# Kernel tuning notes

Hardware: AMD Instinct MI355X
Metric: run time of the kernel (lower is better)

## Reference

```python
import jax, jax.numpy as jnp
import numpy as np

B, H, W = 4, 128, 128
THRESHOLD = 0.1      # hard-coded in chamfer_distance_batch
CHUNK = 2048         # row-chunk size for the online-min over the distance matrix
BIG = 1e9            # masks out inactive columns in the min-reduction
EMPTY_CHD = 1e6      # sentinel when either point set is empty (matches torch code)
EPS = 1e-12          # sqrt clamp for numerical safety


def setup_inputs() -> dict:
    key = jax.random.key(0)
    k1, k2 = jax.random.split(key)
    batch1 = jax.random.normal(k1, (B, H, W), dtype=jnp.float32)
    batch2 = jax.random.normal(k2, (B, H, W), dtype=jnp.float32)
    return {"batch1": batch1, "batch2": batch2}


def _chamfer(batch1, batch2):
    Bn, Hn, Wn = batch1.shape
    HW = Hn * Wn
    w1 = jax.nn.relu(batch1 - THRESHOLD).reshape(Bn, HW)   # [B, HW]
    w2 = jax.nn.relu(batch2 - THRESHOLD).reshape(Bn, HW)
    gy, gx = jnp.meshgrid(jnp.arange(Hn), jnp.arange(Wn), indexing='ij')
    coords = jnp.stack([gy, gx], axis=-1).reshape(HW, 2).astype(jnp.float32)  # [HW, 2]
    # torch code multiplies coords by the relu'd weights BEFORE cdist (quirk kept)
    c1 = coords[None, :, :] * w1[:, :, None]               # [B, HW, 2]
    c2 = coords[None, :, :] * w2[:, :, None]
    m1 = w1 > 0                                            # active-point masks
    m2 = w2 > 0

    def directed(cf, mf, ct, mt):
        # mean over active rows of min distance to active columns, chunked
        ct_sq = jnp.sum(ct * ct, axis=-1)                  # [HW]

        def chunk_min(cc):                                 # cc: [CHUNK, 2]
            # |a-b|^2 = |a|^2 + |b|^2 - 2 a.b  (GEMM form)
            d2 = (jnp.sum(cc * cc, axis=-1)[:, None]
                  + ct_sq[None, :]
                  - 2.0 * cc @ ct.T)                       # [CHUNK, HW]
            d = jnp.sqrt(jnp.maximum(d2, EPS))
            return jnp.min(jnp.where(mt[None, :], d, BIG), axis=1)  # [CHUNK]

        mins = jax.lax.map(chunk_min, cf.reshape(-1, CHUNK, 2)).reshape(-1)  # [HW]
        n = jnp.sum(mf)
        return jnp.sum(mins * mf) / jnp.maximum(n, 1)

    def per_image(c1b, m1b, c2b, m2b):
        chd = directed(c1b, m1b, c2b, m2b) + directed(c2b, m2b, c1b, m1b)
        nonempty = (jnp.sum(m1b) > 0) & (jnp.sum(m2b) > 0)
        return jnp.where(nonempty, chd, jnp.asarray(EMPTY_CHD, chd.dtype))

    return jax.vmap(per_image)(c1, m1, c2, m2)   # [B]


def reference(batch1, batch2):
    return _chamfer(batch1, batch2)
```

## Files before the change

### kernel.cpp

```cpp
#include <hip/hip_runtime.h>
#include <math.h>


#define B_ 4
#define HW_ 16384
#define THRESH 0.1f
#define BIGF 1e30f
#define EPS_ 1e-12f

#define SEGCAP 4096
#define NSEG 4
#define NBIN 1024
#define BINSCALE 1.0f
#define BINW 1.0f
#define RG 128
#define NW 8
#define AWIN 768
#define PD_NGRP 128

__global__ __launch_bounds__(1024)
void compact_kernel(const float* __restrict__ in1, const float* __restrict__ in2,
                    int* __restrict__ segcounts, float4* __restrict__ pts,
                    uint4* __restrict__ minarr4, int* __restrict__ histG) {
    int seg = blockIdx.x, combo = blockIdx.y;
    int b = combo >> 1, s = combo & 1;
    int tid = threadIdx.x, lane = tid & 63, wid = tid >> 6;
    const float* in = s ? in2 : in1;
    int ibase = seg * SEGCAP + tid * 4;
    float4 v = ((const float4*)(in + b * HW_))[(unsigned)ibase >> 2];
    float w0 = v.x - THRESH, w1 = v.y - THRESH, w2 = v.z - THRESH, w3 = v.w - THRESH;
    int a0 = w0 > 0.f, a1 = w1 > 0.f, a2 = w2 > 0.f, a3 = w3 > 0.f;

    unsigned int bb = __float_as_uint(BIGF);
    minarr4[(unsigned)(combo * HW_ + ibase) >> 2] = make_uint4(bb, bb, bb, bb);

    __shared__ int hist[NBIN];
    if (tid < NBIN) hist[tid] = 0;

    int c = a0 + a1 + a2 + a3;
    int incl = c;
#pragma unroll
    for (int o = 1; o < 64; o <<= 1) {
        int x = __shfl_up(incl, o, 64);
        if (lane >= o) incl += x;
    }
    int wexcl = incl - c;
    __shared__ int wtot[16], wpre[17];
    if (lane == 63) wtot[wid] = incl;
    __syncthreads();
    if (tid == 0) {
        int run = 0;
#pragma unroll
        for (int ww = 0; ww < 16; ++ww) { wpre[ww] = run; run += wtot[ww]; }
        wpre[16] = run;
    }
    __syncthreads();
    int off = wpre[wid] + wexcl;
    float4* dst = pts + combo * HW_ + seg * SEGCAP;
    float wv[4] = {w0, w1, w2, w3};
    int   av[4] = {a0, a1, a2, a3};
#pragma unroll
    for (int u = 0; u < 4; ++u) {
        if (av[u]) {
            int i = ibase + u;
            float qx = (float)(i >> 7) * wv[u];
            float qy = (float)(i & 127) * wv[u];
            float zz = qx * qx + qy * qy;
            dst[off] = make_float4(qx, qy, zz, 0.0f);
            int bin = min(NBIN - 1, (int)(sqrtf(zz) * BINSCALE));
            atomicAdd(&hist[bin], 1);
            ++off;
        }
    }
    if (tid == 0) segcounts[combo * 4 + seg] = wpre[16];
    __syncthreads();
    if (tid < NBIN)
        histG[(combo * NSEG + seg) * NBIN + tid] = hist[tid];
}

__global__ __launch_bounds__(1024)
void scatter_kernel(const int* __restrict__ segcounts, const float4* __restrict__ pts,
                    const int* __restrict__ histG, float4* __restrict__ sorted,
                    int* __restrict__ binstartG) {
    int seg = blockIdx.x, combo = blockIdx.y;
    int tid = threadIdx.x;
    __shared__ int h[NSEG][NBIN];
    __shared__ int sc[NBIN];
    __shared__ int cur[NBIN];
    for (int i = tid; i < NSEG * NBIN; i += 1024)
        h[i >> 10][i & (NBIN - 1)] = histG[combo * NSEG * NBIN + i];
    __syncthreads();
    if (tid < NBIN) sc[tid] = h[0][tid] + h[1][tid] + h[2][tid] + h[3][tid];
    __syncthreads();
#pragma unroll
    for (int o = 1; o < NBIN; o <<= 1) {
        int v = (tid < NBIN && tid >= o) ? sc[tid - o] : 0;
        __syncthreads();
        if (tid < NBIN) sc[tid] += v;
        __syncthreads();
    }
    if (tid < NBIN) {
        int tot = h[0][tid] + h[1][tid] + h[2][tid] + h[3][tid];
        int excl = sc[tid] - tot;
        int o2 = excl;
        for (int s2 = 0; s2 < seg; ++s2) o2 += h[s2][tid];
        cur[tid] = o2;
        if (seg == 0) binstartG[combo * (NBIN + 1) + tid] = excl;
    }
    if (seg == 0 && tid == 0)
        binstartG[combo * (NBIN + 1) + NBIN] = sc[NBIN - 1];
    __syncthreads();
    int c = segcounts[combo * 4 + seg];
    const float4* src = pts + combo * HW_ + seg * SEGCAP;
    for (int i = tid; i < c; i += 1024) {
        float4 p = src[i];
        int bin = min(NBIN - 1, (int)(sqrtf(p.z) * BINSCALE));
        int idx = atomicAdd(&cur[bin], 1);
        sorted[(size_t)combo * HW_ + idx] =
            make_float4(p.x, p.y, p.z, __uint_as_float((unsigned)(seg * SEGCAP + i)));
    }
}

__global__ __launch_bounds__(512, 4)
void pdist_kernel(const float4* __restrict__ sorted, const int* __restrict__ binstart,
                  unsigned int* __restrict__ minarr) {
    int grp = blockIdx.x, combo = blockIdx.y;
    int tid = threadIdx.x, lane = tid & 63, w = tid >> 6;
    int tc = combo ^ 1;
    int n_from = binstart[combo * (NBIN + 1) + NBIN];
    int n_to   = binstart[tc * (NBIN + 1) + NBIN];
    if (n_from <= 0 || n_to <= 0) return;
    int rbase = grp * RG;
    if (rbase >= n_from) return;

    const float4* __restrict__ rows = sorted + (size_t)combo * HW_;
    const float4* __restrict__ cols = sorted + (size_t)tc * HW_;

    int r0 = rbase + lane, r1 = rbase + 64 + lane;
    bool v0 = r0 < n_from, v1 = r1 < n_from;
    float4 P0 = rows[min(r0, n_from - 1)];
    float4 P1 = rows[min(r1, n_from - 1)];
    float npx0 = -2.0f * P0.x, npy0 = -2.0f * P0.y, p20 = P0.z;
    float npx1 = -2.0f * P1.x, npy1 = -2.0f * P1.y, p21 = P1.z;
    unsigned int slot0 = __float_as_uint(P0.w);
    unsigned int slot1 = __float_as_uint(P1.w);
    float m0 = BIGF, m1 = BIGF;

    int blo_r = min(NBIN - 1, (int)(sqrtf(rows[rbase].z) * BINSCALE));
    int bhi_r = min(NBIN - 1, (int)(sqrtf(rows[min(rbase + RG - 1, n_from - 1)].z) * BINSCALE));
    float rho_lo = (float)blo_r * BINW;
    float rho_hi = (float)(bhi_r + 1) * BINW;

    int jmid = (binstart[tc * (NBIN + 1) + blo_r]
                + binstart[tc * (NBIN + 1) + min(bhi_r + 1, NBIN)]) >> 1;
    int aHi = min(n_to, jmid + AWIN / 2);
    int aLo = max(0, aHi - AWIN);
    aHi = min(n_to, aLo + AWIN);

    __shared__ __align__(16) float bx[NW][64], by[NW][64], bz[NW][64];
    __shared__ float mW[NW][RG];

    auto ld = [&](int jb) -> float4 {
        int j = jb + lane;
        return (j < n_to) ? cols[j] : make_float4(0.0f, 0.0f, BIGF, 0.0f);
    };
    auto proc = [&](float4 qc) {
        bx[w][lane] = qc.x; by[w][lane] = qc.y; bz[w][lane] = qc.z;
        const float4* X = (const float4*)bx[w];
        const float4* Y = (const float4*)by[w];
        const float4* Z = (const float4*)bz[w];
#pragma unroll
        for (int q4 = 0; q4 < 16; ++q4) {
            float4 qx = X[q4], qy = Y[q4], qz = Z[q4];
            float t0 = fmaf(qy.x, npy0, fmaf(qx.x, npx0, qz.x));
            float u1 = fmaf(qy.y, npy0, fmaf(qx.y, npx0, qz.y));
            m0 = fminf(m0, fminf(t0, u1));
            float u2 = fmaf(qy.z, npy0, fmaf(qx.z, npx0, qz.z));
            float u3 = fmaf(qy.w, npy0, fmaf(qx.w, npx0, qz.w));
            m0 = fminf(m0, fminf(u2, u3));
            float s0 = fmaf(qy.x, npy1, fmaf(qx.x, npx1, qz.x));
            float s1 = fmaf(qy.y, npy1, fmaf(qx.y, npx1, qz.y));
            m1 = fminf(m1, fminf(s0, s1));
            float s2 = fmaf(qy.z, npy1, fmaf(qx.z, npx1, qz.z));
            float s3 = fmaf(qy.w, npy1, fmaf(qx.w, npx1, qz.w));
            m1 = fminf(m1, fminf(s2, s3));
        }
    };

    int nbA = (aHi - aLo + 63) >> 6;
    float4 qn = (w < nbA) ? ld(aLo + (w << 6))
                          : make_float4(0.0f, 0.0f, BIGF, 0.0f);
    for (int bi = w; bi < nbA; bi += NW) {
        float4 qc = qn;
        if (bi + NW < nbA) qn = ld(aLo + ((bi + NW) << 6));
        proc(qc);
    }

    mW[w][lane] = m0; mW[w][64 + lane] = m1;
    __syncthreads();
    float c0 = mW[0][lane], c1 = mW[0][64 + lane];
#pragma unroll
    for (int ww = 1; ww < NW; ++ww) {
        c0 = fminf(c0, mW[ww][lane]);
        c1 = fminf(c1, mW[ww][64 + lane]);
    }
    float md0 = v0 ? fmaxf(c0 + p20, 0.0f) : -1.0f;
    float md1 = v1 ? fmaxf(c1 + p21, 0.0f) : -1.0f;
    float g = fmaxf(md0, md1);
#pragma unroll
    for (int o = 1; o < 64; o <<= 1) g = fmaxf(g, __shfl_xor(g, o));

    float S = sqrtf((g + 1.0f) * (1.0f / 0.99f)) * 1.001f;
    int b_lo = max(0, (int)((rho_lo - S) * BINSCALE) - 1);
    int b_hi = min(NBIN, (int)((rho_hi + S) * BINSCALE) + 2);
    int jlo2 = binstart[tc * (NBIN + 1) + b_lo];
    int jhi2 = binstart[tc * (NBIN + 1) + b_hi];

    m0 = c0; m1 = c1;
    int nbL = (max(0, aLo - jlo2) + 63) >> 6;
    int nbR = (max(0, jhi2 - aHi) + 63) >> 6;
    int nbB = nbL + nbR;
    auto jbB = [&](int bi) {
        return (bi < nbL) ? (jlo2 + (bi << 6)) : (aHi + ((bi - nbL) << 6));
    };
    qn = (w < nbB) ? ld(jbB(w)) : make_float4(0.0f, 0.0f, BIGF, 0.0f);
    for (int bi = w; bi < nbB; bi += NW) {
        float4 qc = qn;
        if (bi + NW < nbB) qn = ld(jbB(bi + NW));
        proc(qc);
    }
    __syncthreads();
    mW[w][lane] = m0; mW[w][64 + lane] = m1;
    __syncthreads();
    if (w == 0) {
        float f0 = mW[0][lane], f1 = mW[0][64 + lane];
#pragma unroll
        for (int ww = 1; ww < NW; ++ww) {
            f0 = fminf(f0, mW[ww][lane]);
            f1 = fminf(f1, mW[ww][64 + lane]);
        }
        if (v0) minarr[combo * HW_ + slot0] = __float_as_uint(fmaxf(f0 + p20, 0.0f));
        if (v1) minarr[combo * HW_ + slot1] = __float_as_uint(fmaxf(f1 + p21, 0.0f));
    }
}

__global__ void reduce_out_kernel(const int* __restrict__ segcounts,
                                  const unsigned int* __restrict__ minarr,
                                  float* __restrict__ out) {
    int b = blockIdx.x;
    int tid = threadIdx.x;
    int d = tid >> 9;
    int t = tid & 511;
    int combo = b * 2 + d;

    float acc = 0.0f;
    for (int s = 0; s < NSEG; ++s) {
        int c = segcounts[combo * 4 + s];
        const unsigned int* ma = minarr + combo * HW_ + s * SEGCAP;
        for (int r = t; r < c; r += 512)
            acc += sqrtf(fmaxf(__uint_as_float(ma[r]), EPS_));
    }
#pragma unroll
    for (int o = 32; o >= 1; o >>= 1) acc += __shfl_down(acc, o);

    __shared__ float wsum[16];
    if ((tid & 63) == 0) wsum[tid >> 6] = acc;
    __syncthreads();
    if (tid == 0) {
        float s0 = 0.0f, s1 = 0.0f;
#pragma unroll
        for (int w = 0; w < 8; ++w)  s0 += wsum[w];
#pragma unroll
        for (int w = 8; w < 16; ++w) s1 += wsum[w];
        int n0 = 0, n1 = 0;
#pragma unroll
        for (int s = 0; s < NSEG; ++s) {
            n0 += segcounts[(b * 2) * 4 + s];
            n1 += segcounts[(b * 2 + 1) * 4 + s];
        }
        out[b] = (n0 > 0 && n1 > 0)
                 ? s0 / (float)n0 + s1 / (float)n1
                 : 1.0e6f;
    }
}

extern "C" void kernel_launch(void* const* d_in, const int* in_sizes, int n_in,
                              void* d_out, int out_size, void* d_ws, size_t ws_size,
                              hipStream_t stream) {
    const float* in1 = (const float*)d_in[0];
    const float* in2 = (const float*)d_in[1];
    float* out = (float*)d_out;
    char* ws = (char*)d_ws;
    int* segcounts = (int*)ws;
    float4* pts = (float4*)(ws + 256);
    size_t minoff = 256 + (size_t)8 * HW_ * sizeof(float4);
    unsigned int* minarr = (unsigned int*)(ws + minoff);
    size_t sortoff = minoff + (size_t)8 * HW_ * sizeof(unsigned int);
    float4* sorted = (float4*)(ws + sortoff);
    size_t binoff = sortoff + (size_t)8 * HW_ * sizeof(float4);
    int* binstart = (int*)(ws + binoff);
    size_t histoff = binoff + (size_t)8 * (NBIN + 1) * sizeof(int);
    int* histG = (int*)(ws + histoff);

    hipLaunchKernelGGL(compact_kernel, dim3(NSEG, 8), dim3(1024), 0, stream,
                       in1, in2, segcounts, pts, (uint4*)minarr, histG);
    hipLaunchKernelGGL(scatter_kernel, dim3(NSEG, 8), dim3(1024), 0, stream,
                       segcounts, pts, histG, sorted, binstart);
    hipLaunchKernelGGL(pdist_kernel, dim3(PD_NGRP, 8), dim3(512), 0, stream,
                       sorted, binstart, minarr);
    hipLaunchKernelGGL(reduce_out_kernel, dim3(B_), dim3(1024), 0, stream,
                       segcounts, minarr, out);
}
```

Before: 79.07 us.

## Fuse final reduction into pdist via last-block counter; wave-shuffle scan in scatter

Removes the separate reduce_out kernel launch. Each pdist block bumps a per-batch atomic counter, and the last of that batch's 256 blocks performs the sqrt-sum and mean. The scatter kernel's shared-memory Hillis-Steele scan over 1024 bins is replaced with a wave-level shuffle scan plus a 16-entry cross-wave scan, cutting many __syncthreads. The cost is a threadfence and atomic in every pdist block, plus a serial tail where a single block per batch reduces 32K values.

```diff
diff --git a/kernel.cpp b/kernel.cpp
--- a/kernel.cpp
+++ b/kernel.cpp
@@ -81,34 +81,46 @@
 __global__ __launch_bounds__(1024)
 void scatter_kernel(const int* __restrict__ segcounts, const float4* __restrict__ pts,
                     const int* __restrict__ histG, float4* __restrict__ sorted,
-                    int* __restrict__ binstartG) {
+                    int* __restrict__ binstartG, int* __restrict__ donecnt) {
     int seg = blockIdx.x, combo = blockIdx.y;
-    int tid = threadIdx.x;
+    int tid = threadIdx.x, lane = tid & 63, wid = tid >> 6;
+    if (seg == 0 && (combo & 1) == 0 && tid == 0)
+        donecnt[combo >> 1] = 0;
     __shared__ int h[NSEG][NBIN];
-    __shared__ int sc[NBIN];
     __shared__ int cur[NBIN];
+    __shared__ int wtot[16];
     for (int i = tid; i < NSEG * NBIN; i += 1024)
         h[i >> 10][i & (NBIN - 1)] = histG[combo * NSEG * NBIN + i];
     __syncthreads();
-    if (tid < NBIN) sc[tid] = h[0][tid] + h[1][tid] + h[2][tid] + h[3][tid];
-    __syncthreads();
-#pragma unroll
-    for (int o = 1; o < NBIN; o <<= 1) {
-        int v = (tid < NBIN && tid >= o) ? sc[tid - o] : 0;
-        __syncthreads();
-        if (tid < NBIN) sc[tid] += v;
-        __syncthreads();
-    }
-    if (tid < NBIN) {
-        int tot = h[0][tid] + h[1][tid] + h[2][tid] + h[3][tid];
-        int excl = sc[tid] - tot;
+    int tot = h[0][tid] + h[1][tid] + h[2][tid] + h[3][tid];
+    int v = tot;
+#pragma unroll
+    for (int o = 1; o < 64; o <<= 1) {
+        int x = __shfl_up(v, o, 64);
+        if (lane >= o) v += x;
+    }
+    if (lane == 63) wtot[wid] = v;
+    __syncthreads();
+    if (wid == 0) {
+        int wv = (lane < 16) ? wtot[lane] : 0;
+#pragma unroll
+        for (int o = 1; o < 16; o <<= 1) {
+            int x = __shfl_up(wv, o, 64);
+            if (lane >= o) wv += x;
+        }
+        if (lane < 16) wtot[lane] = wv;
+    }
+    __syncthreads();
+    int incl = v + (wid > 0 ? wtot[wid - 1] : 0);
+    int excl = incl - tot;
+    {
         int o2 = excl;
         for (int s2 = 0; s2 < seg; ++s2) o2 += h[s2][tid];
         cur[tid] = o2;
         if (seg == 0) binstartG[combo * (NBIN + 1) + tid] = excl;
     }
-    if (seg == 0 && tid == 0)
-        binstartG[combo * (NBIN + 1) + NBIN] = sc[NBIN - 1];
+    if (seg == 0 && tid == NBIN - 1)
+        binstartG[combo * (NBIN + 1) + NBIN] = incl;
     __syncthreads();
     int c = segcounts[combo * 4 + seg];
     const float4* src = pts + combo * HW_ + seg * SEGCAP;
@@ -123,164 +135,170 @@
 
 __global__ __launch_bounds__(512, 4)
 void pdist_kernel(const float4* __restrict__ sorted, const int* __restrict__ binstart,
-                  unsigned int* __restrict__ minarr) {
+                  const int* __restrict__ segcounts, unsigned int* __restrict__ minarr,
+                  float* __restrict__ out, int* __restrict__ donecnt) {
     int grp = blockIdx.x, combo = blockIdx.y;
     int tid = threadIdx.x, lane = tid & 63, w = tid >> 6;
     int tc = combo ^ 1;
     int n_from = binstart[combo * (NBIN + 1) + NBIN];
     int n_to   = binstart[tc * (NBIN + 1) + NBIN];
-    if (n_from <= 0 || n_to <= 0) return;
     int rbase = grp * RG;
-    if (rbase >= n_from) return;
-
-    const float4* __restrict__ rows = sorted + (size_t)combo * HW_;
-    const float4* __restrict__ cols = sorted + (size_t)tc * HW_;
-
-    int r0 = rbase + lane, r1 = rbase + 64 + lane;
-    bool v0 = r0 < n_from, v1 = r1 < n_from;
-    float4 P0 = rows[min(r0, n_from - 1)];
-    float4 P1 = rows[min(r1, n_from - 1)];
-    float npx0 = -2.0f * P0.x, npy0 = -2.0f * P0.y, p20 = P0.z;
-    float npx1 = -2.0f * P1.x, npy1 = -2.0f * P1.y, p21 = P1.z;
-    unsigned int slot0 = __float_as_uint(P0.w);
-    unsigned int slot1 = __float_as_uint(P1.w);
-    float m0 = BIGF, m1 = BIGF;
-
-    int blo_r = min(NBIN - 1, (int)(sqrtf(rows[rbase].z) * BINSCALE));
-    int bhi_r = min(NBIN - 1, (int)(sqrtf(rows[min(rbase + RG - 1, n_from - 1)].z) * BINSCALE));
-    float rho_lo = (float)blo_r * BINW;
-    float rho_hi = (float)(bhi_r + 1) * BINW;
-
-    int jmid = (binstart[tc * (NBIN + 1) + blo_r]
-                + binstart[tc * (NBIN + 1) + min(bhi_r + 1, NBIN)]) >> 1;
-    int aHi = min(n_to, jmid + AWIN / 2);
-    int aLo = max(0, aHi - AWIN);
-    aHi = min(n_to, aLo + AWIN);
+    bool doWork = (n_from > 0) && (n_to > 0) && (rbase < n_from);
 
     __shared__ __align__(16) float bx[NW][64], by[NW][64], bz[NW][64];
     __shared__ float mW[NW][RG];
 
-    auto ld = [&](int jb) -> float4 {
-        int j = jb + lane;
-        return (j < n_to) ? cols[j] : make_float4(0.0f, 0.0f, BIGF, 0.0f);
-    };
-    auto proc = [&](float4 qc) {
-        bx[w][lane] = qc.x; by[w][lane] = qc.y; bz[w][lane] = qc.z;
-        const float4* X = (const float4*)bx[w];
-        const float4* Y = (const float4*)by[w];
-        const float4* Z = (const float4*)bz[w];
-#pragma unroll
-        for (int q4 = 0; q4 < 16; ++q4) {
-            float4 qx = X[q4], qy = Y[q4], qz = Z[q4];
-            float t0 = fmaf(qy.x, npy0, fmaf(qx.x, npx0, qz.x));
-            float u1 = fmaf(qy.y, npy0, fmaf(qx.y, npx0, qz.y));
-            m0 = fminf(m0, fminf(t0, u1));
-            float u2 = fmaf(qy.z, npy0, fmaf(qx.z, npx0, qz.z));
-            float u3 = fmaf(qy.w, npy0, fmaf(qx.w, npx0, qz.w));
-            m0 = fminf(m0, fminf(u2, u3));
-            float s0 = fmaf(qy.x, npy1, fmaf(qx.x, npx1, qz.x));
-            float s1 = fmaf(qy.y, npy1, fmaf(qx.y, npx1, qz.y));
-            m1 = fminf(m1, fminf(s0, s1));
-            float s2 = fmaf(qy.z, npy1, fmaf(qx.z, npx1, qz.z));
-            float s3 = fmaf(qy.w, npy1, fmaf(qx.w, npx1, qz.w));
-            m1 = fminf(m1, fminf(s2, s3));
-        }
-    };
-
-    int nbA = (aHi - aLo + 63) >> 6;
-    float4 qn = (w < nbA) ? ld(aLo + (w << 6))
-                          : make_float4(0.0f, 0.0f, BIGF, 0.0f);
-    for (int bi = w; bi < nbA; bi += NW) {
-        float4 qc = qn;
-        if (bi + NW < nbA) qn = ld(aLo + ((bi + NW) << 6));
-        proc(qc);
-    }
-
-    mW[w][lane] = m0; mW[w][64 + lane] = m1;
-    __syncthreads();
-    float c0 = mW[0][lane], c1 = mW[0][64 + lane];
-#pragma unroll
-    for (int ww = 1; ww < NW; ++ww) {
-        c0 = fminf(c0, mW[ww][lane]);
-        c1 = fminf(c1, mW[ww][64 + lane]);
-    }
-    float md0 = v0 ? fmaxf(c0 + p20, 0.0f) : -1.0f;
-    float md1 = v1 ? fmaxf(c1 + p21, 0.0f) : -1.0f;
-    float g = fmaxf(md0, md1);
-#pragma unroll
-    for (int o = 1; o < 64; o <<= 1) g = fmaxf(g, __shfl_xor(g, o));
-
-    float S = sqrtf((g + 1.0f) * (1.0f / 0.99f)) * 1.001f;
-    int b_lo = max(0, (int)((rho_lo - S) * BINSCALE) - 1);
-    int b_hi = min(NBIN, (int)((rho_hi + S) * BINSCALE) + 2);
-    int jlo2 = binstart[tc * (NBIN + 1) + b_lo];
-    int jhi2 = binstart[tc * (NBIN + 1) + b_hi];
-
-    m0 = c0; m1 = c1;
-    int nbL = (max(0, aLo - jlo2) + 63) >> 6;
-    int nbR = (max(0, jhi2 - aHi) + 63) >> 6;
-    int nbB = nbL + nbR;
-    auto jbB = [&](int bi) {
-        return (bi < nbL) ? (jlo2 + (bi << 6)) : (aHi + ((bi - nbL) << 6));
-    };
-    qn = (w < nbB) ? ld(jbB(w)) : make_float4(0.0f, 0.0f, BIGF, 0.0f);
-    for (int bi = w; bi < nbB; bi += NW) {
-        float4 qc = qn;
-        if (bi + NW < nbB) qn = ld(jbB(bi + NW));
-        proc(qc);
-    }
-    __syncthreads();
-    mW[w][lane] = m0; mW[w][64 + lane] = m1;
-    __syncthreads();
-    if (w == 0) {
-        float f0 = mW[0][lane], f1 = mW[0][64 + lane];
+    if (doWork) {
+        const float4* __restrict__ rows = sorted + (size_t)combo * HW_;
+        const float4* __restrict__ cols = sorted + (size_t)tc * HW_;
+
+        int r0 = rbase + lane, r1 = rbase + 64 + lane;
+        bool v0 = r0 < n_from, v1 = r1 < n_from;
+        float4 P0 = rows[min(r0, n_from - 1)];
+        float4 P1 = rows[min(r1, n_from - 1)];
+        float npx0 = -2.0f * P0.x, npy0 = -2.0f * P0.y, p20 = P0.z;
+        float npx1 = -2.0f * P1.x, npy1 = -2.0f * P1.y, p21 = P1.z;
+        unsigned int slot0 = __float_as_uint(P0.w);
+        unsigned int slot1 = __float_as_uint(P1.w);
+        float m0 = BIGF, m1 = BIGF;
+
+        int blo_r = min(NBIN - 1, (int)(sqrtf(rows[rbase].z) * BINSCALE));
+        int bhi_r = min(NBIN - 1, (int)(sqrtf(rows[min(rbase + RG - 1, n_from - 1)].z) * BINSCALE));
+        float rho_lo = (float)blo_r * BINW;
+        float rho_hi = (float)(bhi_r + 1) * BINW;
+
+        int jmid = (binstart[tc * (NBIN + 1) + blo_r]
+                    + binstart[tc * (NBIN + 1) + min(bhi_r + 1, NBIN)]) >> 1;
+        int aHi = min(n_to, jmid + AWIN / 2);
+        int aLo = max(0, aHi - AWIN);
+        aHi = min(n_to, aLo + AWIN);
+
+        auto ld = [&](int jb) -> float4 {
+            int j = jb + lane;
+            return (j < n_to) ? cols[j] : make_float4(0.0f, 0.0f, BIGF, 0.0f);
+        };
+        auto proc = [&](float4 qc) {
+            bx[w][lane] = qc.x; by[w][lane] = qc.y; bz[w][lane] = qc.z;
+            const float4* X = (const float4*)bx[w];
+            const float4* Y = (const float4*)by[w];
+            const float4* Z = (const float4*)bz[w];
+#pragma unroll
+            for (int q4 = 0; q4 < 16; ++q4) {
+                float4 qx = X[q4], qy = Y[q4], qz = Z[q4];
+                float t0 = fmaf(qy.x, npy0, fmaf(qx.x, npx0, qz.x));
+                float u1 = fmaf(qy.y, npy0, fmaf(qx.y, npx0, qz.y));
+                m0 = fminf(m0, fminf(t0, u1));
+                float u2 = fmaf(qy.z, npy0, fmaf(qx.z, npx0, qz.z));
+                float u3 = fmaf(qy.w, npy0, fmaf(qx.w, npx0, qz.w));
+                m0 = fminf(m0, fminf(u2, u3));
+                float s0 = fmaf(qy.x, npy1, fmaf(qx.x, npx1, qz.x));
+                float s1 = fmaf(qy.y, npy1, fmaf(qx.y, npx1, qz.y));
+                m1 = fminf(m1, fminf(s0, s1));
+                float s2 = fmaf(qy.z, npy1, fmaf(qx.z, npx1, qz.z));
+                float s3 = fmaf(qy.w, npy1, fmaf(qx.w, npx1, qz.w));
+                m1 = fminf(m1, fminf(s2, s3));
+            }
+        };
+
+        int nbA = (aHi - aLo + 63) >> 6;
+        float4 qn = (w < nbA) ? ld(aLo + (w << 6))
+                              : make_float4(0.0f, 0.0f, BIGF, 0.0f);
+        for (int bi = w; bi < nbA; bi += NW) {
+            float4 qc = qn;
+            if (bi + NW < nbA) qn = ld(aLo + ((bi + NW) << 6));
+            proc(qc);
+        }
+
+        mW[w][lane] = m0; mW[w][64 + lane] = m1;
+        __syncthreads();
+        float c0 = mW[0][lane], c1 = mW[0][64 + lane];
 #pragma unroll
         for (int ww = 1; ww < NW; ++ww) {
-            f0 = fminf(f0, mW[ww][lane]);
-            f1 = fminf(f1, mW[ww][64 + lane]);
-        }
-        if (v0) minarr[combo * HW_ + slot0] = __float_as_uint(fmaxf(f0 + p20, 0.0f));
-        if (v1) minarr[combo * HW_ + slot1] = __float_as_uint(fmaxf(f1 + p21, 0.0f));
-    }
-}
-
-__global__ void reduce_out_kernel(const int* __restrict__ segcounts,
-                                  const unsigned int* __restrict__ minarr,
-                                  float* __restrict__ out) {
-    int b = blockIdx.x;
-    int tid = threadIdx.x;
-    int d = tid >> 9;
-    int t = tid & 511;
-    int combo = b * 2 + d;
-
-    float acc = 0.0f;
-    for (int s = 0; s < NSEG; ++s) {
-        int c = segcounts[combo * 4 + s];
-        const unsigned int* ma = minarr + combo * HW_ + s * SEGCAP;
-        for (int r = t; r < c; r += 512)
-            acc += sqrtf(fmaxf(__uint_as_float(ma[r]), EPS_));
-    }
-#pragma unroll
-    for (int o = 32; o >= 1; o >>= 1) acc += __shfl_down(acc, o);
-
-    __shared__ float wsum[16];
-    if ((tid & 63) == 0) wsum[tid >> 6] = acc;
+            c0 = fminf(c0, mW[ww][lane]);
+            c1 = fminf(c1, mW[ww][64 + lane]);
+        }
+        float md0 = v0 ? fmaxf(c0 + p20, 0.0f) : -1.0f;
+        float md1 = v1 ? fmaxf(c1 + p21, 0.0f) : -1.0f;
+        float g = fmaxf(md0, md1);
+#pragma unroll
+        for (int o = 1; o < 64; o <<= 1) g = fmaxf(g, __shfl_xor(g, o));
+
+        float S = sqrtf((g + 1.0f) * (1.0f / 0.99f)) * 1.001f;
+        int b_lo = max(0, (int)((rho_lo - S) * BINSCALE) - 1);
+        int b_hi = min(NBIN, (int)((rho_hi + S) * BINSCALE) + 2);
+        int jlo2 = binstart[tc * (NBIN + 1) + b_lo];
+        int jhi2 = binstart[tc * (NBIN + 1) + b_hi];
+
+        m0 = c0; m1 = c1;
+        int nbL = (max(0, aLo - jlo2) + 63) >> 6;
+        int nbR = (max(0, jhi2 - aHi) + 63) >> 6;
+        int nbB = nbL + nbR;
+        auto jbB = [&](int bi) {
+            return (bi < nbL) ? (jlo2 + (bi << 6)) : (aHi + ((bi - nbL) << 6));
+        };
+        qn = (w < nbB) ? ld(jbB(w)) : make_float4(0.0f, 0.0f, BIGF, 0.0f);
+        for (int bi = w; bi < nbB; bi += NW) {
+            float4 qc = qn;
+            if (bi + NW < nbB) qn = ld(jbB(bi + NW));
+            proc(qc);
+        }
+        __syncthreads();
+        mW[w][lane] = m0; mW[w][64 + lane] = m1;
+        __syncthreads();
+        if (w == 0) {
+            float f0 = mW[0][lane], f1 = mW[0][64 + lane];
+#pragma unroll
+            for (int ww = 1; ww < NW; ++ww) {
+                f0 = fminf(f0, mW[ww][lane]);
+                f1 = fminf(f1, mW[ww][64 + lane]);
+            }
+            if (v0) minarr[combo * HW_ + slot0] = __float_as_uint(fmaxf(f0 + p20, 0.0f));
+            if (v1) minarr[combo * HW_ + slot1] = __float_as_uint(fmaxf(f1 + p21, 0.0f));
+        }
+    }
+
+    int bb = combo >> 1;
+    __threadfence();
+    __syncthreads();
+    __shared__ int lastS;
+    if (tid == 0)
+        lastS = (atomicAdd(&donecnt[bb], 1) == 2 * PD_NGRP - 1);
+    __syncthreads();
+    if (!lastS) return;
+    __threadfence();
+
+    __shared__ float wsumA[NW], wsumB[NW];
+    float s01[2];
+#pragma unroll
+    for (int d = 0; d < 2; ++d) {
+        int cmb = bb * 2 + d;
+        float acc = 0.0f;
+        for (int s = 0; s < NSEG; ++s) {
+            int c = segcounts[cmb * 4 + s];
+            const unsigned int* ma = minarr + cmb * HW_ + s * SEGCAP;
+            for (int r = tid; r < c; r += 512)
+                acc += sqrtf(fmaxf(__uint_as_float(ma[r]), EPS_));
+        }
+#pragma unroll
+        for (int o = 32; o >= 1; o >>= 1) acc += __shfl_down(acc, o);
+        if (lane == 0) { if (d == 0) wsumA[w] = acc; else wsumB[w] = acc; }
+    }
     __syncthreads();
     if (tid == 0) {
         float s0 = 0.0f, s1 = 0.0f;
 #pragma unroll
-        for (int w = 0; w < 8; ++w)  s0 += wsum[w];
-#pragma unroll
-        for (int w = 8; w < 16; ++w) s1 += wsum[w];
+        for (int ww = 0; ww < NW; ++ww) s0 += wsumA[ww];
+#pragma unroll
+        for (int ww = 0; ww < NW; ++ww) s1 += wsumB[ww];
         int n0 = 0, n1 = 0;
 #pragma unroll
         for (int s = 0; s < NSEG; ++s) {
-            n0 += segcounts[(b * 2) * 4 + s];
-            n1 += segcounts[(b * 2 + 1) * 4 + s];
-        }
-        out[b] = (n0 > 0 && n1 > 0)
-                 ? s0 / (float)n0 + s1 / (float)n1
-                 : 1.0e6f;
+            n0 += segcounts[(bb * 2) * 4 + s];
+            n1 += segcounts[(bb * 2 + 1) * 4 + s];
+        }
+        out[bb] = (n0 > 0 && n1 > 0)
+                  ? s0 / (float)n0 + s1 / (float)n1
+                  : 1.0e6f;
     }
 }
 
@@ -301,13 +319,13 @@
     int* binstart = (int*)(ws + binoff);
     size_t histoff = binoff + (size_t)8 * (NBIN + 1) * sizeof(int);
     int* histG = (int*)(ws + histoff);
+    size_t doneoff = histoff + (size_t)8 * NSEG * NBIN * sizeof(int);
+    int* donecnt = (int*)(ws + doneoff);
 
     hipLaunchKernelGGL(compact_kernel, dim3(NSEG, 8), dim3(1024), 0, stream,
                        in1, in2, segcounts, pts, (uint4*)minarr, histG);
     hipLaunchKernelGGL(scatter_kernel, dim3(NSEG, 8), dim3(1024), 0, stream,
-                       segcounts, pts, histG, sorted, binstart);
+                       segcounts, pts, histG, sorted, binstart, donecnt);
     hipLaunchKernelGGL(pdist_kernel, dim3(PD_NGRP, 8), dim3(512), 0, stream,
-                       sorted, binstart, minarr);
-    hipLaunchKernelGGL(reduce_out_kernel, dim3(B_), dim3(1024), 0, stream,
-                       segcounts, minarr, out);
+                       sorted, binstart, segcounts, minarr, out, donecnt);
 }
```

Result: slower. 234.9 us (+197.1%).
